# Kernel tuning notes

Measured on AMD Instinct MI355X. Metric: run time of the kernel, lower is better.

Reference implementation:

```python
import jax, jax.numpy as jnp
import numpy as np

P = 262144
H = 256
EPS = 1e-12  # torch F.normalize eps


def _l2norm(x):
    # matches torch.nn.functional.normalize(x, dim=-1): x / max(||x||, eps)
    n = jnp.linalg.norm(x, axis=-1, keepdims=True)
    return x / jnp.maximum(n, EPS)


def _mlp(x, params):
    # params: list of (W, b); ReLU on all but last layer
    for W, b in params[:-1]:
        x = jax.nn.relu(x @ W + b)
    W, b = params[-1]
    return x @ W + b


def setup_inputs() -> dict:
    key = jax.random.key(0)
    ks = jax.random.split(key, 24)
    inp = {
        "normals": jax.random.normal(ks[0], (P, 3), dtype=jnp.float32),
        "view_dirs": jax.random.normal(ks[1], (P, 3), dtype=jnp.float32),
        "roughness": jax.random.uniform(ks[2], (P, 1), dtype=jnp.float32),
        "r0": jax.random.uniform(ks[3], (P, 1), dtype=jnp.float32),
    }
    # diffuse MLP: 3 -> 256 -> 256 -> 256 -> 3
    d_dims = [3, H, H, H, 3]
    # specular MLP: 8 -> 256 -> 256 -> 256 -> 3
    s_dims = [8, H, H, H, 3]
    k = 4
    for i in range(4):
        fan = d_dims[i]
        inp[f"dW{i}"] = jax.random.normal(ks[k], (d_dims[i], d_dims[i + 1]), dtype=jnp.float32) * (2.0 / fan) ** 0.5
        inp[f"db{i}"] = jnp.zeros((d_dims[i + 1],), dtype=jnp.float32)
        k += 1
    for i in range(4):
        fan = s_dims[i]
        inp[f"sW{i}"] = jax.random.normal(ks[k], (s_dims[i], s_dims[i + 1]), dtype=jnp.float32) * (2.0 / fan) ** 0.5
        inp[f"sb{i}"] = jnp.zeros((s_dims[i + 1],), dtype=jnp.float32)
        k += 1
    return inp


def reference(normals, view_dirs, roughness, r0,
              dW0, db0, dW1, db1, dW2, db2, dW3, db3,
              sW0, sb0, sW1, sb1, sW2, sb2, sW3, sb3):
    n = _l2norm(normals)
    v = _l2norm(view_dirs)
    inputs_specular = jnp.concatenate((n, v, roughness, r0), axis=-1)  # [P,8]
    visible = (n * v).sum(axis=-1) > 0  # [P]
    d_params = [(dW0, db0), (dW1, db1), (dW2, db2), (dW3, db3)]
    s_params = [(sW0, sb0), (sW1, sb1), (sW2, sb2), (sW3, sb3)]
    # Faithful to gather->MLP->scatter-into-zeros: pointwise MLP computed
    # everywhere, non-visible rows zeroed (identical math, static shapes).
    mask = visible[:, None]
    diffuse_rgb = jnp.where(mask, _mlp(n, d_params), 0.0)
    specular_rgb = jnp.where(mask, _mlp(inputs_specular, s_params), 0.0)
    return (diffuse_rgb, specular_rgb)
```

## Files before the change

### kernel.cpp

```cpp
#include <hip/hip_runtime.h>

typedef _Float16 f16;
typedef _Float16 f16x8 __attribute__((ext_vector_type(8)));
typedef __fp16   fp16x2 __attribute__((ext_vector_type(2)));
typedef float    f32x16 __attribute__((ext_vector_type(16)));
typedef float    f32x4  __attribute__((ext_vector_type(4)));
typedef unsigned int u32;
typedef unsigned int u32x4 __attribute__((ext_vector_type(4)));

#define NPTS 262144

#define NET_F16   143360
#define BIAS_BYTE 573440

static __device__ __forceinline__ u32 pkrtz(float a, float b) {
    fp16x2 h = __builtin_amdgcn_cvt_pkrtz(a, b);
    return __builtin_bit_cast(u32, h);
}
static __device__ __forceinline__ u32 relu_pk(float a, float b) {
    return pkrtz(fmaxf(a, 0.0f), fmaxf(b, 0.0f));
}

__global__ void prep_kernel(
    const float* __restrict__ dW0, const float* __restrict__ db0,
    const float* __restrict__ dW1, const float* __restrict__ db1,
    const float* __restrict__ dW2, const float* __restrict__ db2,
    const float* __restrict__ dW3, const float* __restrict__ db3,
    const float* __restrict__ sW0, const float* __restrict__ sb0,
    const float* __restrict__ sW1, const float* __restrict__ sb1,
    const float* __restrict__ sW2, const float* __restrict__ sb2,
    const float* __restrict__ sW3, const float* __restrict__ sb3,
    f16* __restrict__ wpk, float* __restrict__ bpk)
{
    const int ROWS = 17920;
    int t = blockIdx.x * 256 + threadIdx.x;
    if (t < 2 * ROWS) {
        int net = (t >= ROWS) ? 1 : 0;
        int r = t - net * ROWS;
        const float* W0 = net ? sW0 : dW0;
        const float* W1 = net ? sW1 : dW1;
        const float* W2 = net ? sW2 : dW2;
        const float* W3 = net ? sW3 : dW3;
        int K0 = net ? 8 : 3;
        f16* o = wpk + net * NET_F16;
        if (r < 512) {
            int lane = r & 63;
            int m  = 32 * (r >> 6) + (lane & 31);
            int kb = 8 * (lane >> 5);
            f16* q = o + r * 8;
            #pragma unroll
            for (int j = 0; j < 8; ++j) {
                int k = kb + j;
                q[j] = (f16)((k < K0) ? W0[k * 256 + m] : 0.0f);
            }
        } else if (r < 512 + 8192) {
            int rr = r - 512;
            int lane = rr & 63;
            int hh = lane >> 5;
            int m  = 32 * ((rr >> 6) & 7) + (lane & 31);
            int kt = rr >> 9;
            f16* q = o + 4096 + rr * 8;
            #pragma unroll
            for (int j = 0; j < 8; ++j) {
                int kp = 32 * (kt >> 1) + 16 * (kt & 1) + (j & 3) + 8 * (j >> 2) + 4 * hh;
                q[j] = (f16)W1[kp * 256 + m];
            }
        } else if (r < 512 + 16384) {
            int rr = r - (512 + 8192);
            int lane = rr & 63;
            int hh = lane >> 5;
            int m  = 32 * ((rr >> 6) & 7) + (lane & 31);
            int kt = rr >> 9;
            f16* q = o + 69632 + rr * 8;
            #pragma unroll
            for (int j = 0; j < 8; ++j) {
                int kp = 32 * (kt >> 1) + 16 * (kt & 1) + (j & 3) + 8 * (j >> 2) + 4 * hh;
                q[j] = (f16)W2[kp * 256 + m];
            }
        } else {
            int rr = r - (512 + 16384);
            int lane = rr & 63;
            int hh = lane >> 5;
            int m  = lane & 31;
            int kt = rr >> 6;
            f16* q = o + 135168 + rr * 8;
            #pragma unroll
            for (int j = 0; j < 8; ++j) {
                int kp = 32 * (kt >> 1) + 16 * (kt & 1) + (j & 3) + 8 * (j >> 2) + 4 * hh;
                q[j] = (f16)((m < 3) ? W3[kp * 3 + m] : 0.0f);
            }
        }
    } else if (t < 2 * ROWS + 1600) {
        int tb = t - 2 * ROWS;
        int net = (tb >= 800) ? 1 : 0;
        int i = tb - net * 800;
        float val;
        if (i < 768) {
            int layer = i >> 8;
            const float* bl = net ? (layer == 0 ? sb0 : layer == 1 ? sb1 : sb2)
                                  : (layer == 0 ? db0 : layer == 1 ? db1 : db2);
            int q  = i & 255;
            int rg = q & 15, h = (q >> 4) & 1;
            int m  = 32 * (q >> 5) + (rg & 3) + 8 * (rg >> 2) + 4 * h;
            val = bl[m];
        } else {
            int q  = i - 768;
            int rg = q & 15, h = q >> 4;
            int m  = (rg & 3) + 8 * (rg >> 2) + 4 * h;
            const float* b3 = net ? sb3 : db3;
            val = (m < 3) ? b3[m] : 0.0f;
        }
        bpk[net * 800 + i] = val;
    }
}

#define WAITB(WS) do {                                                          \
    asm volatile("s_waitcnt vmcnt(" WS ") lgkmcnt(0)" ::: "memory");            \
    __builtin_amdgcn_sched_barrier(0);                                          \
    __builtin_amdgcn_s_barrier();                                               \
    __builtin_amdgcn_sched_barrier(0);                                          \
} while (0)

#define STAGE1(S, C0) do {                                                      \
    const u32x4* g_ = ws + (C0) * 512 + woff + lane;                            \
    u32x4* l_ = &ring[S][woff];                                                 \
    __builtin_amdgcn_global_load_lds(                                           \
        (const __attribute__((address_space(1))) void*)g_,                      \
        (__attribute__((address_space(3))) void*)l_, 16, 0, 0);                 \
    __builtin_amdgcn_global_load_lds(                                           \
        (const __attribute__((address_space(1))) void*)(g_ + 64),               \
        (__attribute__((address_space(3))) void*)(l_ + 64), 16, 0, 0);          \
} while (0)
#define STAGE2(S, C0) do {                                                      \
    _Pragma("unroll")                                                           \
    for (int i_ = 0; i_ < 2; ++i_) {                                            \
        const u32x4* g_ = ws + ((C0) + i_) * 512 + woff + lane;                 \
        u32x4* l_ = &ring[S][i_ * 512 + woff];                                  \
        __builtin_amdgcn_global_load_lds(                                       \
            (const __attribute__((address_space(1))) void*)g_,                  \
            (__attribute__((address_space(3))) void*)l_, 16, 0, 0);             \
        __builtin_amdgcn_global_load_lds(                                       \
            (const __attribute__((address_space(1))) void*)(g_ + 64),           \
            (__attribute__((address_space(3))) void*)(l_ + 64), 16, 0, 0);      \
    }                                                                           \
} while (0)

#define CHUNK256(S, CI, KT) do {                                                \
    const u32x4* bq_ = &ring[S][(CI) * 512];                                    \
    const f16x8 xh_ = __builtin_bit_cast(f16x8, xf[KT]);                        \
    _Pragma("unroll")                                                           \
    for (int mt_ = 0; mt_ < 8; ++mt_) {                                         \
        const f16x8 a_ = __builtin_bit_cast(f16x8, bq_[mt_ * 64 + lane]);       \
        acc[mt_] = __builtin_amdgcn_mfma_f32_32x32x16_f16(a_, xh_, acc[mt_], 0, 0, 0); \
    }                                                                           \
} while (0)

#define BINIT(dst, boff) do {                                                   \
    const f32x4* b4_ = (const f32x4*)(biasl + (boff) + hi * 16);                \
    const f32x4 v0_ = b4_[0], v1_ = b4_[1], v2_ = b4_[2], v3_ = b4_[3];         \
    _Pragma("unroll")                                                           \
    for (int j = 0; j < 4; ++j) {                                               \
        (dst)[j] = v0_[j]; (dst)[4 + j] = v1_[j];                               \
        (dst)[8 + j] = v2_[j]; (dst)[12 + j] = v3_[j];                          \
    }                                                                           \
} while (0)

#define EPI() do {                                                              \
    _Pragma("unroll")                                                           \
    for (int mt = 0; mt < 8; ++mt) {                                            \
        _Pragma("unroll")                                                       \
        for (int q = 0; q < 2; ++q) {                                           \
            u32x4 w;                                                            \
            w[0] = relu_pk(acc[mt][8*q+0], acc[mt][8*q+1]);                     \
            w[1] = relu_pk(acc[mt][8*q+2], acc[mt][8*q+3]);                     \
            w[2] = relu_pk(acc[mt][8*q+4], acc[mt][8*q+5]);                     \
            w[3] = relu_pk(acc[mt][8*q+6], acc[mt][8*q+7]);                     \
            xf[2*mt+q] = w;                                                     \
        }                                                                       \
    }                                                                           \
} while (0)

__launch_bounds__(256, 2)
__global__ void mlp_kernel(const float* __restrict__ gn, const float* __restrict__ gv,
                           const float* __restrict__ gro, const float* __restrict__ gr0,
                           const f16* __restrict__ wpk, const float* __restrict__ bpk,
                           float* __restrict__ out)
{
    __shared__ u32x4 ring[3][1024];
    __shared__ __align__(16) float biasl[1600];

    const int tid  = threadIdx.x;
    const int wv   = tid >> 6;
    const int lane = tid & 63;
    const int l32  = lane & 31;
    const int hi   = lane >> 5;
    const int p    = blockIdx.x * 128 + wv * 32 + l32;
    const int woff = wv * 128;
    const u32x4* ws = (const u32x4*)wpk;

    biasl[tid]        = bpk[tid];
    biasl[tid + 256]  = bpk[tid + 256];
    biasl[tid + 512]  = bpk[tid + 512];
    biasl[tid + 768]  = bpk[tid + 768];
    biasl[tid + 1024] = bpk[tid + 1024];
    biasl[tid + 1280] = bpk[tid + 1280];
    if (tid < 64) biasl[tid + 1536] = bpk[tid + 1536];

    u32x4 xd = {0,0,0,0}, xs = {0,0,0,0};
    bool vis = false;
    if (hi == 0) {
        float nx = gn[3*p], ny = gn[3*p+1], nz = gn[3*p+2];
        float vx = gv[3*p], vy = gv[3*p+1], vz = gv[3*p+2];
        float ro = gro[p], rr = gr0[p];
        float ni = 1.0f / fmaxf(sqrtf(nx*nx + ny*ny + nz*nz), 1e-12f);
        float vi = 1.0f / fmaxf(sqrtf(vx*vx + vy*vy + vz*vz), 1e-12f);
        nx *= ni; ny *= ni; nz *= ni; vx *= vi; vy *= vi; vz *= vi;
        vis = (nx*vx + ny*vy + nz*vz) > 0.0f;
        xd[0] = pkrtz(nx, ny); xd[1] = pkrtz(nz, 0.0f);
        xs[0] = xd[0];         xs[1] = pkrtz(nz, vx);
        xs[2] = pkrtz(vy, vz); xs[3] = pkrtz(ro, rr);
    }

    __syncthreads();

    STAGE1(0, 0);
    STAGE2(1, 1);

    f32x16 acc[8];
    u32x4  xf[16];

    #pragma unroll
    for (int net = 0; net < 2; ++net) {
        const int cb = net * 35;
        const int bb = net * 800;
        const f16x8 xh0 = __builtin_bit_cast(f16x8, net ? xs : xd);

        WAITB("4");
        STAGE2(2, cb + 3);
        {
            const u32x4* bufq = &ring[0][0];
            #pragma unroll
            for (int mt = 0; mt < 8; ++mt) {
                f32x16 ci;
                BINIT(ci, bb + mt * 32);
                const f16x8 a = __builtin_bit_cast(f16x8, bufq[mt * 64 + lane]);
                acc[mt] = __builtin_amdgcn_mfma_f32_32x32x16_f16(a, xh0, ci, 0, 0, 0);
            }
        }
        EPI();

        #pragma unroll
        for (int mt = 0; mt < 8; ++mt) BINIT(acc[mt], bb + 256 + mt * 32);
        #pragma unroll
        for (int t = 1; t <= 8; ++t) {
            WAITB("4");
            STAGE2((t + 2) % 3, cb + 2 * t + 3);
            CHUNK256(t % 3, 0, 2 * t - 2);
            CHUNK256(t % 3, 1, 2 * t - 1);
        }
        EPI();

        #pragma unroll
        for (int mt = 0; mt < 8; ++mt) BINIT(acc[mt], bb + 512 + mt * 32);
        #pragma unroll
        for (int t = 9; t <= 15; ++t) {
            WAITB("4");
            STAGE2((t + 2) % 3, cb + 2 * t + 3);
            CHUNK256(t % 3, 0, 2 * t - 18);
            CHUNK256(t % 3, 1, 2 * t - 17);
        }
        WAITB("4");
        if (net == 0) STAGE1(0, 35);
        CHUNK256(16 % 3, 0, 14);
        CHUNK256(16 % 3, 1, 15);
        EPI();

        if (net == 0) { WAITB("2"); STAGE2(1, 36); }
        else          { WAITB("0"); }
        {
            f32x16 c3;
            BINIT(c3, bb + 768);
            const u32x4* bq0 = &ring[2][0];
            const u32x4* bq1 = &ring[2][512];
            #pragma unroll
            for (int i = 0; i < 8; ++i) {
                const f16x8 a = __builtin_bit_cast(f16x8, bq0[i * 64 + lane]);
                c3 = __builtin_amdgcn_mfma_f32_32x32x16_f16(a, __builtin_bit_cast(f16x8, xf[i]), c3, 0, 0, 0);
            }
            #pragma unroll
            for (int i = 0; i < 8; ++i) {
                const f16x8 a = __builtin_bit_cast(f16x8, bq1[i * 64 + lane]);
                c3 = __builtin_amdgcn_mfma_f32_32x32x16_f16(a, __builtin_bit_cast(f16x8, xf[8 + i]), c3, 0, 0, 0);
            }
            if (hi == 0) {
                float* op = out + net * (NPTS * 3) + p * 3;
                op[0] = vis ? c3[0] : 0.0f;
                op[1] = vis ? c3[1] : 0.0f;
                op[2] = vis ? c3[2] : 0.0f;
            }
        }
    }
}

extern "C" void kernel_launch(void* const* d_in, const int* in_sizes, int n_in,
                              void* d_out, int out_size, void* d_ws, size_t ws_size,
                              hipStream_t stream)
{
    f16*   wpk = (f16*)d_ws;
    float* bpk = (float*)((char*)d_ws + BIAS_BYTE);

    prep_kernel<<<147, 256, 0, stream>>>(
        (const float*)d_in[4],  (const float*)d_in[5],
        (const float*)d_in[6],  (const float*)d_in[7],
        (const float*)d_in[8],  (const float*)d_in[9],
        (const float*)d_in[10], (const float*)d_in[11],
        (const float*)d_in[12], (const float*)d_in[13],
        (const float*)d_in[14], (const float*)d_in[15],
        (const float*)d_in[16], (const float*)d_in[17],
        (const float*)d_in[18], (const float*)d_in[19],
        wpk, bpk);

    mlp_kernel<<<2048, 256, 0, stream>>>(
        (const float*)d_in[0], (const float*)d_in[1],
        (const float*)d_in[2], (const float*)d_in[3],
        wpk, bpk, (float*)d_out);
}
```

Before: 149.0 us.

## Read MLP weights directly from global memory instead of LDS ring buffer

Removes the triple-buffered LDS ring that staged weight chunks via global_load_lds with per-chunk waitcnt plus barrier. Every wave now loads its MFMA A-operand weight fragments straight from global memory, relying on L1/L2 caching because all blocks share the same weights. This drops the block-wide barriers and the 48KB of LDS, which may allow more resident blocks. In exchange, each wave issues its own global loads, so weight traffic through the caches grows fourfold per block, and load latency is no longer hidden by explicit prefetching.

```diff
diff --git a/kernel.cpp b/kernel.cpp
--- a/kernel.cpp
+++ b/kernel.cpp
@@ -114,43 +114,12 @@
     }
 }
 
-#define WAITB(WS) do {                                                          \
-    asm volatile("s_waitcnt vmcnt(" WS ") lgkmcnt(0)" ::: "memory");            \
-    __builtin_amdgcn_sched_barrier(0);                                          \
-    __builtin_amdgcn_s_barrier();                                               \
-    __builtin_amdgcn_sched_barrier(0);                                          \
-} while (0)
-
-#define STAGE1(S, C0) do {                                                      \
-    const u32x4* g_ = ws + (C0) * 512 + woff + lane;                            \
-    u32x4* l_ = &ring[S][woff];                                                 \
-    __builtin_amdgcn_global_load_lds(                                           \
-        (const __attribute__((address_space(1))) void*)g_,                      \
-        (__attribute__((address_space(3))) void*)l_, 16, 0, 0);                 \
-    __builtin_amdgcn_global_load_lds(                                           \
-        (const __attribute__((address_space(1))) void*)(g_ + 64),               \
-        (__attribute__((address_space(3))) void*)(l_ + 64), 16, 0, 0);          \
-} while (0)
-#define STAGE2(S, C0) do {                                                      \
-    _Pragma("unroll")                                                           \
-    for (int i_ = 0; i_ < 2; ++i_) {                                            \
-        const u32x4* g_ = ws + ((C0) + i_) * 512 + woff + lane;                 \
-        u32x4* l_ = &ring[S][i_ * 512 + woff];                                  \
-        __builtin_amdgcn_global_load_lds(                                       \
-            (const __attribute__((address_space(1))) void*)g_,                  \
-            (__attribute__((address_space(3))) void*)l_, 16, 0, 0);             \
-        __builtin_amdgcn_global_load_lds(                                       \
-            (const __attribute__((address_space(1))) void*)(g_ + 64),           \
-            (__attribute__((address_space(3))) void*)(l_ + 64), 16, 0, 0);      \
-    }                                                                           \
-} while (0)
-
-#define CHUNK256(S, CI, KT) do {                                                \
-    const u32x4* bq_ = &ring[S][(CI) * 512];                                    \
+#define CHUNK256_D(C, KT) do {                                                  \
+    const u32x4* wq_ = ws + (C) * 512 + lane;                                   \
     const f16x8 xh_ = __builtin_bit_cast(f16x8, xf[KT]);                        \
     _Pragma("unroll")                                                           \
     for (int mt_ = 0; mt_ < 8; ++mt_) {                                         \
-        const f16x8 a_ = __builtin_bit_cast(f16x8, bq_[mt_ * 64 + lane]);       \
+        const f16x8 a_ = __builtin_bit_cast(f16x8, wq_[mt_ * 64]);              \
         acc[mt_] = __builtin_amdgcn_mfma_f32_32x32x16_f16(a_, xh_, acc[mt_], 0, 0, 0); \
     }                                                                           \
 } while (0)
@@ -186,7 +155,6 @@
                            const f16* __restrict__ wpk, const float* __restrict__ bpk,
                            float* __restrict__ out)
 {
-    __shared__ u32x4 ring[3][1024];
     __shared__ __align__(16) float biasl[1600];
 
     const int tid  = threadIdx.x;
@@ -195,7 +163,6 @@
     const int l32  = lane & 31;
     const int hi   = lane >> 5;
     const int p    = blockIdx.x * 128 + wv * 32 + l32;
-    const int woff = wv * 128;
     const u32x4* ws = (const u32x4*)wpk;
 
     biasl[tid]        = bpk[tid];
@@ -223,9 +190,6 @@
 
     __syncthreads();
 
-    STAGE1(0, 0);
-    STAGE2(1, 1);
-
     f32x16 acc[8];
     u32x4  xf[16];
 
@@ -235,15 +199,13 @@
         const int bb = net * 800;
         const f16x8 xh0 = __builtin_bit_cast(f16x8, net ? xs : xd);
 
-        WAITB("4");
-        STAGE2(2, cb + 3);
         {
-            const u32x4* bufq = &ring[0][0];
+            const u32x4* wq = ws + cb * 512 + lane;
             #pragma unroll
             for (int mt = 0; mt < 8; ++mt) {
                 f32x16 ci;
                 BINIT(ci, bb + mt * 32);
-                const f16x8 a = __builtin_bit_cast(f16x8, bufq[mt * 64 + lane]);
+                const f16x8 a = __builtin_bit_cast(f16x8, wq[mt * 64]);
                 acc[mt] = __builtin_amdgcn_mfma_f32_32x32x16_f16(a, xh0, ci, 0, 0, 0);
             }
         }
@@ -252,44 +214,28 @@
         #pragma unroll
         for (int mt = 0; mt < 8; ++mt) BINIT(acc[mt], bb + 256 + mt * 32);
         #pragma unroll
-        for (int t = 1; t <= 8; ++t) {
-            WAITB("4");
-            STAGE2((t + 2) % 3, cb + 2 * t + 3);
-            CHUNK256(t % 3, 0, 2 * t - 2);
-            CHUNK256(t % 3, 1, 2 * t - 1);
-        }
+        for (int kt = 0; kt < 16; ++kt) CHUNK256_D(cb + 1 + kt, kt);
         EPI();
 
         #pragma unroll
         for (int mt = 0; mt < 8; ++mt) BINIT(acc[mt], bb + 512 + mt * 32);
         #pragma unroll
-        for (int t = 9; t <= 15; ++t) {
-            WAITB("4");
-            STAGE2((t + 2) % 3, cb + 2 * t + 3);
-            CHUNK256(t % 3, 0, 2 * t - 18);
-            CHUNK256(t % 3, 1, 2 * t - 17);
-        }
-        WAITB("4");
-        if (net == 0) STAGE1(0, 35);
-        CHUNK256(16 % 3, 0, 14);
-        CHUNK256(16 % 3, 1, 15);
+        for (int kt = 0; kt < 16; ++kt) CHUNK256_D(cb + 17 + kt, kt);
         EPI();
 
-        if (net == 0) { WAITB("2"); STAGE2(1, 36); }
-        else          { WAITB("0"); }
         {
             f32x16 c3;
             BINIT(c3, bb + 768);
-            const u32x4* bq0 = &ring[2][0];
-            const u32x4* bq1 = &ring[2][512];
+            const u32x4* bq0 = ws + (cb + 33) * 512 + lane;
+            const u32x4* bq1 = ws + (cb + 34) * 512 + lane;
             #pragma unroll
             for (int i = 0; i < 8; ++i) {
-                const f16x8 a = __builtin_bit_cast(f16x8, bq0[i * 64 + lane]);
+                const f16x8 a = __builtin_bit_cast(f16x8, bq0[i * 64]);
                 c3 = __builtin_amdgcn_mfma_f32_32x32x16_f16(a, __builtin_bit_cast(f16x8, xf[i]), c3, 0, 0, 0);
             }
             #pragma unroll
             for (int i = 0; i < 8; ++i) {
-                const f16x8 a = __builtin_bit_cast(f16x8, bq1[i * 64 + lane]);
+                const f16x8 a = __builtin_bit_cast(f16x8, bq1[i * 64]);
                 c3 = __builtin_amdgcn_mfma_f32_32x32x16_f16(a, __builtin_bit_cast(f16x8, xf[8 + i]), c3, 0, 0, 0);
             }
             if (hi == 0) {
```

After: 329.0 us. 2.21x slower.

## Stage three weight chunks per barrier and flatten both MLPs into one pipeline

Applied to the files above, without the earlier changes.

The LDS ring buffer now holds three 256-wide weight chunks per slot instead of two, and each slot is filled by a three-chunk async global-to-LDS load. Both MLPs run as one explicitly unrolled chunk schedule, so prefetching carries across the diffuse-to-specular boundary. The aim is fewer block barriers and waits per chunk of MFMA work, and less pipeline stall between the two networks. In exchange LDS use per block rises by about half, which could limit the two-blocks-per-CU occupancy, and the code is much longer.

```diff
diff --git a/kernel.cpp b/kernel.cpp
--- a/kernel.cpp
+++ b/kernel.cpp
@@ -121,19 +121,9 @@
     __builtin_amdgcn_sched_barrier(0);                                          \
 } while (0)
 
-#define STAGE1(S, C0) do {                                                      \
-    const u32x4* g_ = ws + (C0) * 512 + woff + lane;                            \
-    u32x4* l_ = &ring[S][woff];                                                 \
-    __builtin_amdgcn_global_load_lds(                                           \
-        (const __attribute__((address_space(1))) void*)g_,                      \
-        (__attribute__((address_space(3))) void*)l_, 16, 0, 0);                 \
-    __builtin_amdgcn_global_load_lds(                                           \
-        (const __attribute__((address_space(1))) void*)(g_ + 64),               \
-        (__attribute__((address_space(3))) void*)(l_ + 64), 16, 0, 0);          \
-} while (0)
-#define STAGE2(S, C0) do {                                                      \
-    _Pragma("unroll")                                                           \
-    for (int i_ = 0; i_ < 2; ++i_) {                                            \
+#define STAGE3(S, C0) do {                                                      \
+    _Pragma("unroll")                                                           \
+    for (int i_ = 0; i_ < 3; ++i_) {                                            \
         const u32x4* g_ = ws + ((C0) + i_) * 512 + woff + lane;                 \
         u32x4* l_ = &ring[S][i_ * 512 + woff];                                  \
         __builtin_amdgcn_global_load_lds(                                       \
@@ -144,9 +134,19 @@
             (__attribute__((address_space(3))) void*)(l_ + 64), 16, 0, 0);      \
     }                                                                           \
 } while (0)
-
-#define CHUNK256(S, CI, KT) do {                                                \
-    const u32x4* bq_ = &ring[S][(CI) * 512];                                    \
+#define STAGE_LAST() do {                                                       \
+    const u32x4* g_ = ws + 69 * 512 + woff + lane;                              \
+    u32x4* l_ = &ring[2][woff];                                                 \
+    __builtin_amdgcn_global_load_lds(                                           \
+        (const __attribute__((address_space(1))) void*)g_,                      \
+        (__attribute__((address_space(3))) void*)l_, 16, 0, 0);                 \
+    __builtin_amdgcn_global_load_lds(                                           \
+        (const __attribute__((address_space(1))) void*)(g_ + 64),               \
+        (__attribute__((address_space(3))) void*)(l_ + 64), 16, 0, 0);          \
+} while (0)
+
+#define CHW(C, KT) do {                                                         \
+    const u32x4* bq_ = &ring[((C) / 3) % 3][((C) % 3) * 512];                   \
     const f16x8 xh_ = __builtin_bit_cast(f16x8, xf[KT]);                        \
     _Pragma("unroll")                                                           \
     for (int mt_ = 0; mt_ < 8; ++mt_) {                                         \
@@ -155,6 +155,27 @@
     }                                                                           \
 } while (0)
 
+#define L3W(C, HB) do {                                                         \
+    const u32x4* bq_ = &ring[((C) / 3) % 3][((C) % 3) * 512];                   \
+    _Pragma("unroll")                                                           \
+    for (int i_ = 0; i_ < 8; ++i_) {                                            \
+        const f16x8 a_ = __builtin_bit_cast(f16x8, bq_[i_ * 64 + lane]);        \
+        c3 = __builtin_amdgcn_mfma_f32_32x32x16_f16(                            \
+                a_, __builtin_bit_cast(f16x8, xf[(HB) + i_]), c3, 0, 0, 0);     \
+    }                                                                           \
+} while (0)
+
+#define L0W(C, BB, XH) do {                                                     \
+    const u32x4* bq_ = &ring[((C) / 3) % 3][((C) % 3) * 512];                   \
+    _Pragma("unroll")                                                           \
+    for (int mt_ = 0; mt_ < 8; ++mt_) {                                         \
+        f32x16 ci_;                                                             \
+        BINIT(ci_, (BB) + mt_ * 32);                                            \
+        const f16x8 a_ = __builtin_bit_cast(f16x8, bq_[mt_ * 64 + lane]);       \
+        acc[mt_] = __builtin_amdgcn_mfma_f32_32x32x16_f16(a_, XH, ci_, 0, 0, 0);\
+    }                                                                           \
+} while (0)
+
 #define BINIT(dst, boff) do {                                                   \
     const f32x4* b4_ = (const f32x4*)(biasl + (boff) + hi * 16);                \
     const f32x4 v0_ = b4_[0], v1_ = b4_[1], v2_ = b4_[2], v3_ = b4_[3];         \
@@ -163,6 +184,11 @@
         (dst)[j] = v0_[j]; (dst)[4 + j] = v1_[j];                               \
         (dst)[8 + j] = v2_[j]; (dst)[12 + j] = v3_[j];                          \
     }                                                                           \
+} while (0)
+
+#define BINIT_ALL(boff) do {                                                    \
+    _Pragma("unroll")                                                           \
+    for (int mt = 0; mt < 8; ++mt) BINIT(acc[mt], (boff) + mt * 32);            \
 } while (0)
 
 #define EPI() do {                                                              \
@@ -186,7 +212,7 @@
                            const f16* __restrict__ wpk, const float* __restrict__ bpk,
                            float* __restrict__ out)
 {
-    __shared__ u32x4 ring[3][1024];
+    __shared__ u32x4 ring[3][1536];
     __shared__ __align__(16) float biasl[1600];
 
     const int tid  = threadIdx.x;
@@ -223,81 +249,71 @@
 
     __syncthreads();
 
-    STAGE1(0, 0);
-    STAGE2(1, 1);
+    STAGE3(0, 0);
+    STAGE3(1, 3);
 
     f32x16 acc[8];
     u32x4  xf[16];
-
-    #pragma unroll
-    for (int net = 0; net < 2; ++net) {
-        const int cb = net * 35;
-        const int bb = net * 800;
-        const f16x8 xh0 = __builtin_bit_cast(f16x8, net ? xs : xd);
-
-        WAITB("4");
-        STAGE2(2, cb + 3);
-        {
-            const u32x4* bufq = &ring[0][0];
-            #pragma unroll
-            for (int mt = 0; mt < 8; ++mt) {
-                f32x16 ci;
-                BINIT(ci, bb + mt * 32);
-                const f16x8 a = __builtin_bit_cast(f16x8, bufq[mt * 64 + lane]);
-                acc[mt] = __builtin_amdgcn_mfma_f32_32x32x16_f16(a, xh0, ci, 0, 0, 0);
-            }
+    const f16x8 xh0 = __builtin_bit_cast(f16x8, xd);
+    const f16x8 xh1 = __builtin_bit_cast(f16x8, xs);
+
+    WAITB("6"); STAGE3(2, 6);
+    L0W(0, 0, xh0); EPI(); BINIT_ALL(256);
+    CHW(1, 0); CHW(2, 1);
+    WAITB("6"); STAGE3(0, 9);  CHW(3, 2);  CHW(4, 3);  CHW(5, 4);
+    WAITB("6"); STAGE3(1, 12); CHW(6, 5);  CHW(7, 6);  CHW(8, 7);
+    WAITB("6"); STAGE3(2, 15); CHW(9, 8);  CHW(10, 9); CHW(11, 10);
+    WAITB("6"); STAGE3(0, 18); CHW(12, 11); CHW(13, 12); CHW(14, 13);
+    WAITB("6"); STAGE3(1, 21);
+    CHW(15, 14); CHW(16, 15); EPI(); BINIT_ALL(512);
+    CHW(17, 0);
+    WAITB("6"); STAGE3(2, 24); CHW(18, 1);  CHW(19, 2);  CHW(20, 3);
+    WAITB("6"); STAGE3(0, 27); CHW(21, 4);  CHW(22, 5);  CHW(23, 6);
+    WAITB("6"); STAGE3(1, 30); CHW(24, 7);  CHW(25, 8);  CHW(26, 9);
+    WAITB("6"); STAGE3(2, 33); CHW(27, 10); CHW(28, 11); CHW(29, 12);
+    WAITB("6"); STAGE3(0, 36);
+    CHW(30, 13); CHW(31, 14); CHW(32, 15); EPI();
+    WAITB("6"); STAGE3(1, 39);
+    {
+        f32x16 c3;
+        BINIT(c3, 768);
+        L3W(33, 0);
+        L3W(34, 8);
+        if (hi == 0) {
+            float* op = out + p * 3;
+            op[0] = vis ? c3[0] : 0.0f;
+            op[1] = vis ? c3[1] : 0.0f;
+            op[2] = vis ? c3[2] : 0.0f;
         }
-        EPI();
-
-        #pragma unroll
-        for (int mt = 0; mt < 8; ++mt) BINIT(acc[mt], bb + 256 + mt * 32);
-        #pragma unroll
-        for (int t = 1; t <= 8; ++t) {
-            WAITB("4");
-            STAGE2((t + 2) % 3, cb + 2 * t + 3);
-            CHUNK256(t % 3, 0, 2 * t - 2);
-            CHUNK256(t % 3, 1, 2 * t - 1);
-        }
-        EPI();
-
-        #pragma unroll
-        for (int mt = 0; mt < 8; ++mt) BINIT(acc[mt], bb + 512 + mt * 32);
-        #pragma unroll
-        for (int t = 9; t <= 15; ++t) {
-            WAITB("4");
-            STAGE2((t + 2) % 3, cb + 2 * t + 3);
-            CHUNK256(t % 3, 0, 2 * t - 18);
-            CHUNK256(t % 3, 1, 2 * t - 17);
-        }
-        WAITB("4");
-        if (net == 0) STAGE1(0, 35);
-        CHUNK256(16 % 3, 0, 14);
-        CHUNK256(16 % 3, 1, 15);
-        EPI();
-
-        if (net == 0) { WAITB("2"); STAGE2(1, 36); }
-        else          { WAITB("0"); }
-        {
-            f32x16 c3;
-            BINIT(c3, bb + 768);
-            const u32x4* bq0 = &ring[2][0];
-            const u32x4* bq1 = &ring[2][512];
-            #pragma unroll
-            for (int i = 0; i < 8; ++i) {
-                const f16x8 a = __builtin_bit_cast(f16x8, bq0[i * 64 + lane]);
-                c3 = __builtin_amdgcn_mfma_f32_32x32x16_f16(a, __builtin_bit_cast(f16x8, xf[i]), c3, 0, 0, 0);
-            }
-            #pragma unroll
-            for (int i = 0; i < 8; ++i) {
-                const f16x8 a = __builtin_bit_cast(f16x8, bq1[i * 64 + lane]);
-                c3 = __builtin_amdgcn_mfma_f32_32x32x16_f16(a, __builtin_bit_cast(f16x8, xf[8 + i]), c3, 0, 0, 0);
-            }
-            if (hi == 0) {
-                float* op = out + net * (NPTS * 3) + p * 3;
-                op[0] = vis ? c3[0] : 0.0f;
-                op[1] = vis ? c3[1] : 0.0f;
-                op[2] = vis ? c3[2] : 0.0f;
-            }
+    }
+    L0W(35, 800, xh1); EPI(); BINIT_ALL(800 + 256);
+
+    WAITB("6"); STAGE3(2, 42); CHW(36, 0);  CHW(37, 1);  CHW(38, 2);
+    WAITB("6"); STAGE3(0, 45); CHW(39, 3);  CHW(40, 4);  CHW(41, 5);
+    WAITB("6"); STAGE3(1, 48); CHW(42, 6);  CHW(43, 7);  CHW(44, 8);
+    WAITB("6"); STAGE3(2, 51); CHW(45, 9);  CHW(46, 10); CHW(47, 11);
+    WAITB("6"); STAGE3(0, 54); CHW(48, 12); CHW(49, 13); CHW(50, 14);
+    WAITB("6"); STAGE3(1, 57);
+    CHW(51, 15); EPI(); BINIT_ALL(800 + 512);
+    CHW(52, 0); CHW(53, 1);
+    WAITB("6"); STAGE3(2, 60); CHW(54, 2);  CHW(55, 3);  CHW(56, 4);
+    WAITB("6"); STAGE3(0, 63); CHW(57, 5);  CHW(58, 6);  CHW(59, 7);
+    WAITB("6"); STAGE3(1, 66); CHW(60, 8);  CHW(61, 9);  CHW(62, 10);
+    WAITB("6"); STAGE_LAST();
+    CHW(63, 11); CHW(64, 12); CHW(65, 13);
+    WAITB("2");
+    {
+        CHW(66, 14); CHW(67, 15); EPI();
+        f32x16 c3;
+        BINIT(c3, 800 + 768);
+        L3W(68, 0);
+        WAITB("0");
+        L3W(69, 8);
+        if (hi == 0) {
+            float* op = out + NPTS * 3 + p * 3;
+            op[0] = vis ? c3[0] : 0.0f;
+            op[1] = vis ? c3[1] : 0.0f;
+            op[2] = vis ? c3[2] : 0.0f;
         }
     }
 }
```

Result: no change. 147.6 us (-0.9%).
